# Optimization experiments

Hardware: AMD Instinct MI355X
Metric: run time of the kernel (lower is better)

The kernel has to match this reference:

```python
import jax, jax.numpy as jnp
import numpy as np
import math

B, N, D, H, O = 2, 1024, 256, 4, 8
DT, STEPS = 0.1, 5


def setup_inputs() -> dict:
    key = jax.random.key(0)
    ks = jax.random.split(key, 8)
    inv_d = 1.0 / math.sqrt(D)
    inv_ho = 1.0 / math.sqrt(H * O)
    return {
        "x": jax.random.normal(ks[0], (B, N, D), jnp.float32),
        "Wq": jax.random.normal(ks[1], (D, D), jnp.float32) * inv_d,
        "Wk": jax.random.normal(ks[2], (D, D), jnp.float32) * inv_d,
        "Wp": jax.random.normal(ks[3], (H * O, D), jnp.float32) * inv_d,
        "bp": jnp.zeros((H * O,), jnp.float32),
        "Wo": jax.random.normal(ks[4], (D, H * O), jnp.float32) * inv_ho,
        "bo": jnp.zeros((D,), jnp.float32),
        "omega": jax.random.normal(ks[5], (H, O), jnp.float32) * 0.1,
        "coupling_scale": jnp.asarray(1.0, jnp.float32),
    }


def reference(x, Wq, Wk, Wp, bp, Wo, bo, omega, coupling_scale):
    dk = D // H
    # attention coupling J_ij = softmax(q_i.k_j / sqrt(d_k))  -> (B,H,N,N)
    q = (x @ Wq.T).reshape(B, N, H, dk).transpose(0, 2, 1, 3)
    k = (x @ Wk.T).reshape(B, N, H, dk).transpose(0, 2, 1, 3)
    J = jax.nn.softmax(jnp.einsum('bhid,bhjd->bhij', q, k) / math.sqrt(dk), axis=-1)
    # initial phases (B,H,N,O)
    phases = (x @ Wp.T + bp).reshape(B, N, H, O).transpose(0, 2, 1, 3)
    om = omega[None, :, None, :]  # (1,H,1,O)

    def step(ph, _):
        # sum_j J_ij sin(phi_j - phi_i) = cos(phi_i)*(J@sin phi) - sin(phi_i)*(J@cos phi)
        s, c = jnp.sin(ph), jnp.cos(ph)
        coupling = c * jnp.einsum('bhij,bhjo->bhio', J, s) - s * jnp.einsum('bhij,bhjo->bhio', J, c)
        new = ph + DT * (om + coupling_scale * coupling)
        new = jnp.remainder(new + jnp.pi, 2 * jnp.pi) - jnp.pi
        return new, None

    phases, _ = jax.lax.scan(step, phases, None, length=STEPS)
    sig = jnp.cos(phases).transpose(0, 2, 1, 3).reshape(B, N, H * O)
    return sig @ Wo.T + bo
```

## Files before the change

kernel.cpp:

```cpp
#include <hip/hip_runtime.h>
#include <hip/hip_bf16.h>
#include <math.h>


#define NB 1024
#define NH 4
#define DD 256
#define NO 8
#define SCSZ 131072
#define PI_F      3.14159265358979323846f
#define TWO_PI_F  6.28318530717958647692f
#define INV_2PI_F 0.15915494309189533577f

typedef __attribute__((ext_vector_type(8))) short bf16x8;
typedef __attribute__((ext_vector_type(4))) float f32x4;
typedef unsigned long long u64;

__device__ __forceinline__ float b2f_u(unsigned short s) {
    union { unsigned u; float f; } x; x.u = ((unsigned)s) << 16; return x.f;
}
__device__ __forceinline__ unsigned short f2b(float f) {
    union { float f; unsigned u; } v; v.f = f;
    unsigned r = v.u + 0x7FFFu + ((v.u >> 16) & 1u);
    return (unsigned short)(r >> 16);
}
template<bool F32>
__device__ __forceinline__ uint4 load_pack8(const void* p, size_t off) {
    if (!F32) return *(const uint4*)((const unsigned short*)p + off);
    const float* fp = (const float*)p + off;
    float4 a = *(const float4*)fp;
    float4 b = *(const float4*)(fp + 4);
    uint4 r;
    r.x = (unsigned)f2b(a.x) | ((unsigned)f2b(a.y) << 16);
    r.y = (unsigned)f2b(a.z) | ((unsigned)f2b(a.w) << 16);
    r.z = (unsigned)f2b(b.x) | ((unsigned)f2b(b.y) << 16);
    r.w = (unsigned)f2b(b.z) | ((unsigned)f2b(b.w) << 16);
    return r;
}
__device__ __forceinline__ void load8_rt(int f32, const void* p, int i, float* f) {
    if (f32) {
        const float* fp = (const float*)p + i;
        float4 a = *(const float4*)fp;
        float4 b = *(const float4*)(fp + 4);
        f[0]=a.x; f[1]=a.y; f[2]=a.z; f[3]=a.w;
        f[4]=b.x; f[5]=b.y; f[6]=b.z; f[7]=b.w;
    } else {
        uint4 u = *(const uint4*)((const unsigned short*)p + i);
        f[0] = b2f_u(u.x & 0xFFFFu); f[1] = b2f_u(u.x >> 16);
        f[2] = b2f_u(u.y & 0xFFFFu); f[3] = b2f_u(u.y >> 16);
        f[4] = b2f_u(u.z & 0xFFFFu); f[5] = b2f_u(u.z >> 16);
        f[6] = b2f_u(u.w & 0xFFFFu); f[7] = b2f_u(u.w >> 16);
    }
}
__device__ __forceinline__ float read_cs_bf16(const void* p) {
    float vb = b2f_u(*(const unsigned short*)p);
    bool ok = isfinite(vb) && fabsf(vb) > 1e-30f && fabsf(vb) < 1e30f;
    if (ok) return vb;
    return *(const float*)p;
}
__device__ __forceinline__ int detect_inline(const unsigned short* x) {
    int l = threadIdx.x & 63;
    float a0 = fabsf(b2f_u(x[2 * l]));
    float a1 = fabsf(b2f_u(x[2 * (l + 64)]));
    unsigned long long b0 = __ballot(!(a0 >= 1e-10f && a0 <= 100.0f));
    unsigned long long b1 = __ballot(!(a1 >= 1e-10f && a1 <= 100.0f));
    return (__popcll(b0) + __popcll(b1)) > 16;
}
__device__ __forceinline__ void st8_llc(void* p, u64 v) {
    __hip_atomic_store((u64*)p, v, __ATOMIC_RELAXED, __HIP_MEMORY_SCOPE_AGENT);
}
__device__ __forceinline__ void st4_llc(unsigned* p, unsigned v) {
    __hip_atomic_store(p, v, __ATOMIC_RELAXED, __HIP_MEMORY_SCOPE_AGENT);
}
__device__ __forceinline__ void wait_flags64(const unsigned* f, unsigned tgt) {
    const int l = threadIdx.x & 63;
    unsigned spins = 0;
    for (;;) {
        unsigned v = __hip_atomic_load(f + l, __ATOMIC_RELAXED,
                                       __HIP_MEMORY_SCOPE_AGENT);
        if (__all((int)(v >= tgt))) break;
        __builtin_amdgcn_s_sleep(1);
        if (++spins > (1u << 18)) break;
    }
}
__device__ __forceinline__ void wait_flags_batch(const unsigned* f, unsigned tgt) {
    const int l = threadIdx.x & 63;
    unsigned spins = 0;
    for (;;) {
        unsigned a = __hip_atomic_load(f + l,       __ATOMIC_RELAXED, __HIP_MEMORY_SCOPE_AGENT);
        unsigned b = __hip_atomic_load(f + 64 + l,  __ATOMIC_RELAXED, __HIP_MEMORY_SCOPE_AGENT);
        unsigned c = __hip_atomic_load(f + 128 + l, __ATOMIC_RELAXED, __HIP_MEMORY_SCOPE_AGENT);
        unsigned d = __hip_atomic_load(f + 192 + l, __ATOMIC_RELAXED, __HIP_MEMORY_SCOPE_AGENT);
        unsigned m = min(min(a, b), min(c, d));
        if (__all((int)(m >= tgt))) break;
        __builtin_amdgcn_s_sleep(1);
        if (++spins > (1u << 18)) break;
    }
}

template<bool F32>
__device__ void projm_impl(
    const void* __restrict__ x, const void* __restrict__ Wq,
    const void* __restrict__ Wk, const void* __restrict__ Wp,
    const void* __restrict__ bp,
    unsigned short* __restrict__ Qb, unsigned short* __restrict__ Kb,
    float* __restrict__ PH, unsigned short* __restrict__ SC)
{
    __shared__ uint4 Xsh[64 * 32];
    __shared__ uint4 Wsh[64 * 32];
    const int tid = threadIdx.x;
    const int ftile = blockIdx.x % 9, itile = blockIdx.x / 9;
    const int i0 = itile * 64, f0 = ftile * 64;
    const int wave = tid >> 6, lane = tid & 63;
    const int n = lane & 15, quad = lane >> 4;

    #pragma unroll
    for (int g = 0; g < 8; g++) {
        int fidx = g * 256 + tid;
        int row = fidx >> 5, q = fidx & 31;
        int sw = (q & 24) | ((q ^ row) & 7);
        Xsh[row * 32 + sw] = load_pack8<F32>(x, (size_t)(i0 + row) * 256 + q * 8);
        int wr = f0 + row;
        uint4 wv = make_uint4(0, 0, 0, 0);
        if (wr < 256)      wv = load_pack8<F32>(Wq, (size_t)wr * 256 + q * 8);
        else if (wr < 512) wv = load_pack8<F32>(Wk, (size_t)(wr - 256) * 256 + q * 8);
        else if (wr < 544) wv = load_pack8<F32>(Wp, (size_t)(wr - 512) * 256 + q * 8);
        Wsh[row * 32 + sw] = wv;
    }
    __syncthreads();

    f32x4 acc[4];
    #pragma unroll
    for (int s = 0; s < 4; s++) acc[s] = (f32x4){0.f, 0.f, 0.f, 0.f};
    const int xrow = wave * 16 + n;
    #pragma unroll
    for (int s = 0; s < 8; s++) {
        int qc = s * 4 + quad;
        bf16x8 b = ((const bf16x8*)Xsh)[xrow * 32 + ((qc & 24) | ((qc ^ xrow) & 7))];
        #pragma unroll
        for (int sub = 0; sub < 4; sub++) {
            int wr = sub * 16 + n;
            bf16x8 a = ((const bf16x8*)Wsh)[wr * 32 + ((qc & 24) | ((qc ^ wr) & 7))];
            acc[sub] = __builtin_amdgcn_mfma_f32_16x16x32_bf16(a, b, acc[sub], 0, 0, 0);
        }
    }

    const int ig = i0 + wave * 16 + n;
    const int bb = ig >> 10, nr = ig & 1023;
    if (ftile < 4) {
        #pragma unroll
        for (int sub = 0; sub < 4; sub++) {
            int dd = sub * 16 + quad * 4;
            ushort4 v = make_ushort4(f2b(acc[sub][0] * 0.125f), f2b(acc[sub][1] * 0.125f),
                                     f2b(acc[sub][2] * 0.125f), f2b(acc[sub][3] * 0.125f));
            *(ushort4*)(Qb + ((size_t)((bb * NH + ftile) * NB + nr)) * 64 + dd) = v;
        }
    } else if (ftile < 8) {
        int h = ftile - 4;
        #pragma unroll
        for (int sub = 0; sub < 4; sub++) {
            int dd = sub * 16 + quad * 4;
            ushort4 v = make_ushort4(f2b(acc[sub][0]), f2b(acc[sub][1]),
                                     f2b(acc[sub][2]), f2b(acc[sub][3]));
            *(ushort4*)(Kb + ((size_t)((bb * NH + h) * NB + nr)) * 64 + dd) = v;
        }
    } else {
        #pragma unroll
        for (int sub = 0; sub < 2; sub++) {
            #pragma unroll
            for (int r = 0; r < 4; r++) {
                int fp = sub * 16 + quad * 4 + r;
                int h2 = fp >> 3, o = fp & 7;
                float bpv = F32 ? ((const float*)bp)[fp]
                                : b2f_u(((const unsigned short*)bp)[fp]);
                float v = acc[sub][r] + bpv;
                int bh = bb * NH + h2;
                PH[(size_t)bh * 8192 + o * 1024 + nr] = v;
                float sv, cv;
                __sincosf(v, &sv, &cv);
                SC[(size_t)(bh * 16 + o) * 1024 + nr]     = f2b(sv);
                SC[(size_t)(bh * 16 + 8 + o) * 1024 + nr] = f2b(cv);
            }
        }
    }
}

__global__ __launch_bounds__(256) void k_projm(
    const unsigned short* x, const void* Wq, const void* Wk, const void* Wp,
    const void* bp, unsigned short* Qb, unsigned short* Kb, float* PH,
    unsigned short* SC, unsigned int* flg)
{
    if (blockIdx.x == 0) {
        flg[threadIdx.x] = 0u;
        flg[threadIdx.x + 256] = 0u;
    }
    if (detect_inline(x)) projm_impl<true >(x, Wq, Wk, Wp, bp, Qb, Kb, PH, SC);
    else                  projm_impl<false>(x, Wq, Wk, Wp, bp, Qb, Kb, PH, SC);
}

__global__ __launch_bounds__(256) void k_mega4(
    const unsigned short* __restrict__ xraw,
    const unsigned short* __restrict__ Qb, const unsigned short* __restrict__ Kb,
    const float* __restrict__ PH0,
    unsigned short* __restrict__ SCB,
    const void* __restrict__ omega, const void* __restrict__ csp,
    const void* __restrict__ Wo, const void* __restrict__ bo,
    void* __restrict__ out, unsigned int* __restrict__ flg)
{
    __shared__ uint4 Ush[16 * 128];
    __shared__ f32x4 red[4][64];
    __shared__ float redS[4][16];
    __shared__ float Rsh[16];
    __shared__ float sig[4][32];

    const int tid = threadIdx.x;
    const int bid = blockIdx.x;
    const int bh  = bid >> 6;
    const int i0  = (bid & 63) * 16;
    const int wave = tid >> 6, lane = tid & 63;
    const int n = lane & 15, quad = lane >> 4;
    const int f32 = detect_inline(xraw);

    const unsigned short* qrow = Qb + ((size_t)(bh * NB) + i0 + n) * 64;
    bf16x8 bq0 = *(const bf16x8*)(qrow + quad * 8);
    bf16x8 bq1 = *(const bf16x8*)(qrow + 32 + quad * 8);
    float s = 0.f;
    const unsigned short* kbase = Kb + ((size_t)(bh * NB) + n) * 64;
    #pragma unroll
    for (int t = 0; t < 16; t++) {
        int jt = wave * 16 + t;
        const unsigned short* arow = kbase + (size_t)jt * 16 * 64;
        bf16x8 a0 = *(const bf16x8*)(arow + quad * 8);
        bf16x8 a1 = *(const bf16x8*)(arow + 32 + quad * 8);
        f32x4 acc = {0.f, 0.f, 0.f, 0.f};
        acc = __builtin_amdgcn_mfma_f32_16x16x32_bf16(a0, bq0, acc, 0, 0, 0);
        acc = __builtin_amdgcn_mfma_f32_16x16x32_bf16(a1, bq1, acc, 0, 0, 0);
        float u0 = __expf(acc[0]);
        float u1 = __expf(acc[1]);
        float u2 = __expf(acc[2]);
        float u3 = __expf(acc[3]);
        s += (u0 + u1) + (u2 + u3);
        ushort4 uv = make_ushort4(f2b(u0), f2b(u1), f2b(u2), f2b(u3));
        int cw = 2 * jt + (quad >> 1);
        ((ushort4*)Ush)[(n * 128 + (cw ^ (n & 7))) * 2 + (quad & 1)] = uv;
    }
    s += __shfl_xor(s, 16);
    s += __shfl_xor(s, 32);
    if (lane < 16) redS[wave][lane] = s;
    __syncthreads();
    if (tid < 16)
        Rsh[tid] = 1.0f / (redS[0][tid] + redS[1][tid] + redS[2][tid] + redS[3][tid]);

    float P[4];
    float cs_ = 0.f, om_ = 0.f;
    if (wave == 0 && n < 8) {
        const int o = n, h = bh & 3;
        cs_ = f32 ? *(const float*)csp : read_cs_bf16(csp);
        om_ = f32 ? ((const float*)omega)[h * NO + o]
                  : b2f_u(((const unsigned short*)omega)[h * NO + o]);
        float4 pv = *(const float4*)(PH0 + (size_t)bh * 8192 + o * 1024 + i0 + quad * 4);
        P[0] = pv.x; P[1] = pv.y; P[2] = pv.z; P[3] = pv.w;
    }

    #pragma unroll 1
    for (int k = 0; k < 5; k++) {
        const unsigned short* scrow = SCB + (size_t)k * SCSZ + (size_t)(bh * 16 + n) * 1024;
        unsigned short* scout       = SCB + (size_t)(k + 1) * SCSZ;
        f32x4 acc = {0.f, 0.f, 0.f, 0.f};
        #pragma unroll
        for (int t = 0; t < 8; t++) {
            int it = wave * 8 + t;
            bf16x8 a = ((const bf16x8*)Ush)[n * 128 + ((it * 4 + quad) ^ (n & 7))];
            bf16x8 b = *(const bf16x8*)(scrow + it * 32 + quad * 8);
            acc = __builtin_amdgcn_mfma_f32_16x16x32_bf16(a, b, acc, 0, 0, 0);
        }
        red[wave][lane] = acc;
        __syncthreads();

        if (wave == 0) {
            f32x4 a0 = red[0][lane], a1 = red[1][lane];
            f32x4 a2 = red[2][lane], a3 = red[3][lane];
            #pragma unroll
            for (int v = 0; v < 4; v++) acc[v] = (a0[v] + a1[v]) + (a2[v] + a3[v]);
            float C0 = __shfl_xor(acc[0], 8);
            float C1 = __shfl_xor(acc[1], 8);
            float C2 = __shfl_xor(acc[2], 8);
            float C3 = __shfl_xor(acc[3], 8);
            if (n < 8) {
                const int o = n;
                float S[4] = {acc[0], acc[1], acc[2], acc[3]};
                float C[4] = {C0, C1, C2, C3};
                float Rr[4] = {Rsh[quad * 4], Rsh[quad * 4 + 1],
                               Rsh[quad * 4 + 2], Rsh[quad * 4 + 3]};
                unsigned short sb[4], cb[4];
                #pragma unroll
                for (int r = 0; r < 4; r++) {
                    float si, ci;
                    __sincosf(P[r], &si, &ci);
                    float coup = (ci * S[r] - si * C[r]) * Rr[r];
                    float v = P[r] + 0.1f * (om_ + cs_ * coup);
                    float t2 = v + PI_F;
                    t2 -= floorf(t2 * INV_2PI_F) * TWO_PI_F;
                    P[r] = t2 - PI_F;
                    float sn, cn;
                    __sincosf(P[r], &sn, &cn);
                    sb[r] = f2b(sn); cb[r] = f2b(cn);
                }
                u64 sv = (u64)sb[0] | ((u64)sb[1] << 16) | ((u64)sb[2] << 32) | ((u64)sb[3] << 48);
                u64 cv = (u64)cb[0] | ((u64)cb[1] << 16) | ((u64)cb[2] << 32) | ((u64)cb[3] << 48);
                int i = i0 + quad * 4;
                st8_llc(scout + (size_t)(bh * 16 + o) * 1024 + i,     sv);
                st8_llc(scout + (size_t)(bh * 16 + 8 + o) * 1024 + i, cv);
            }
        }
        __syncthreads();
        if (tid == 0) st4_llc(&flg[bid], (unsigned)(k + 1));
        if (k < 4) {
            if (wave == 0) wait_flags64(&flg[bh * 64], (unsigned)(k + 1));
        } else {
            if (wave == 0) wait_flags_batch(&flg[(bid >> 8) * 256], 5u);
        }
        __syncthreads();
    }

    const unsigned short* scfin = SCB + (size_t)5 * SCSZ;
    const int ob = bid >> 8, n0 = (bid & 255) * 4;
    if (tid < 32) {
        int h = tid >> 3, o = tid & 7;
        u64 q = *(const u64*)(scfin + (size_t)((ob * NH + h) * 16 + 8 + o) * 1024 + n0);
        #pragma unroll
        for (int r = 0; r < 4; r++)
            sig[r][tid] = b2f_u((unsigned short)(q >> (16 * r)));
    }
    __syncthreads();
    float wv[32];
    #pragma unroll
    for (int d0 = 0; d0 < 32; d0 += 8) load8_rt(f32, Wo, tid * 32 + d0, wv + d0);
    const float bov = f32 ? ((const float*)bo)[tid] : b2f_u(((const unsigned short*)bo)[tid]);
    #pragma unroll
    for (int r = 0; r < 4; r++) {
        float acc = bov;
        #pragma unroll
        for (int t = 0; t < 32; t++) acc += sig[r][t] * wv[t];
        size_t oi = ((size_t)ob * 1024 + n0 + r) * DD + tid;
        if (f32) ((float*)out)[oi] = acc;
        else     ((unsigned short*)out)[oi] = f2b(acc);
    }
}

extern "C" void kernel_launch(void* const* d_in, const int* in_sizes, int n_in,
                              void* d_out, int out_size, void* d_ws, size_t ws_size,
                              hipStream_t stream)
{
    const unsigned short* x = (const unsigned short*)d_in[0];
    const void* Wq  = d_in[1];
    const void* Wk  = d_in[2];
    const void* Wp  = d_in[3];
    const void* bp  = d_in[4];
    const void* Wo  = d_in[5];
    const void* bo  = d_in[6];
    const void* om  = d_in[7];
    const void* cs  = d_in[8];

    char* w = (char*)d_ws;
    unsigned short* Qb  = (unsigned short*)w;
    unsigned short* Kb  = (unsigned short*)(w + (1u << 20));
    float*          PH0 = (float*)(w + (2u << 20));
    unsigned short* SCB = (unsigned short*)(w + (2u << 20) + (256u << 10));
    unsigned int*   flg = (unsigned int*)(w + (4u << 20));

    k_projm<<<288, 256, 0, stream>>>(x, Wq, Wk, Wp, bp, Qb, Kb, PH0, SCB, flg);
    k_mega4<<<512, 256, 0, stream>>>(x, Qb, Kb, PH0, SCB, om, cs,
                                     Wo, bo, d_out, flg);
}
```

Before: 127.3 us.

## Split output projection into separate kernel and streamline per-step flag sync

Moves the final output projection out of the persistent step kernel into a new k_out launch, so the last step no longer needs a grid-wide flag wait and can use plain stores. The per-step barrier now waits on vmcnt and has one lane publish the flag, polling inside the step branch instead of bracketing it with extra __syncthreads. This trades a software global barrier for an extra kernel launch boundary.

```diff
diff --git a/kernel.cpp b/kernel.cpp
--- a/kernel.cpp
+++ b/kernel.cpp
@@ -79,20 +79,6 @@
         unsigned v = __hip_atomic_load(f + l, __ATOMIC_RELAXED,
                                        __HIP_MEMORY_SCOPE_AGENT);
         if (__all((int)(v >= tgt))) break;
-        __builtin_amdgcn_s_sleep(1);
-        if (++spins > (1u << 18)) break;
-    }
-}
-__device__ __forceinline__ void wait_flags_batch(const unsigned* f, unsigned tgt) {
-    const int l = threadIdx.x & 63;
-    unsigned spins = 0;
-    for (;;) {
-        unsigned a = __hip_atomic_load(f + l,       __ATOMIC_RELAXED, __HIP_MEMORY_SCOPE_AGENT);
-        unsigned b = __hip_atomic_load(f + 64 + l,  __ATOMIC_RELAXED, __HIP_MEMORY_SCOPE_AGENT);
-        unsigned c = __hip_atomic_load(f + 128 + l, __ATOMIC_RELAXED, __HIP_MEMORY_SCOPE_AGENT);
-        unsigned d = __hip_atomic_load(f + 192 + l, __ATOMIC_RELAXED, __HIP_MEMORY_SCOPE_AGENT);
-        unsigned m = min(min(a, b), min(c, d));
-        if (__all((int)(m >= tgt))) break;
         __builtin_amdgcn_s_sleep(1);
         if (++spins > (1u << 18)) break;
     }
@@ -204,14 +190,12 @@
     const float* __restrict__ PH0,
     unsigned short* __restrict__ SCB,
     const void* __restrict__ omega, const void* __restrict__ csp,
-    const void* __restrict__ Wo, const void* __restrict__ bo,
-    void* __restrict__ out, unsigned int* __restrict__ flg)
+    unsigned int* __restrict__ flg)
 {
     __shared__ uint4 Ush[16 * 128];
     __shared__ f32x4 red[4][64];
     __shared__ float redS[4][16];
     __shared__ float Rsh[16];
-    __shared__ float sig[4][32];
 
     const int tid = threadIdx.x;
     const int bid = blockIdx.x;
@@ -309,19 +293,31 @@
                 u64 sv = (u64)sb[0] | ((u64)sb[1] << 16) | ((u64)sb[2] << 32) | ((u64)sb[3] << 48);
                 u64 cv = (u64)cb[0] | ((u64)cb[1] << 16) | ((u64)cb[2] << 32) | ((u64)cb[3] << 48);
                 int i = i0 + quad * 4;
-                st8_llc(scout + (size_t)(bh * 16 + o) * 1024 + i,     sv);
-                st8_llc(scout + (size_t)(bh * 16 + 8 + o) * 1024 + i, cv);
+                u64* ps = (u64*)(scout + (size_t)(bh * 16 + o) * 1024 + i);
+                u64* pc = (u64*)(scout + (size_t)(bh * 16 + 8 + o) * 1024 + i);
+                if (k < 4) { st8_llc(ps, sv); st8_llc(pc, cv); }
+                else       { *ps = sv;        *pc = cv; }
             }
-        }
-        __syncthreads();
-        if (tid == 0) st4_llc(&flg[bid], (unsigned)(k + 1));
-        if (k < 4) {
-            if (wave == 0) wait_flags64(&flg[bh * 64], (unsigned)(k + 1));
-        } else {
-            if (wave == 0) wait_flags_batch(&flg[(bid >> 8) * 256], 5u);
-        }
-        __syncthreads();
-    }
+            if (k < 4) {
+                asm volatile("s_waitcnt vmcnt(0)" ::: "memory");
+                if (lane == 0) st4_llc(&flg[bid], (unsigned)(k + 1));
+                wait_flags64(flg + bh * 64, (unsigned)(k + 1));
+            }
+        }
+        if (k < 4) __syncthreads();
+    }
+}
+
+__global__ __launch_bounds__(256) void k_out(
+    const unsigned short* __restrict__ xraw,
+    const unsigned short* __restrict__ SCB,
+    const void* __restrict__ Wo, const void* __restrict__ bo,
+    void* __restrict__ out)
+{
+    __shared__ float sig[4][32];
+    const int tid = threadIdx.x;
+    const int bid = blockIdx.x;
+    const int f32 = detect_inline(xraw);
 
     const unsigned short* scfin = SCB + (size_t)5 * SCSZ;
     const int ob = bid >> 8, n0 = (bid & 255) * 4;
@@ -370,6 +366,6 @@
     unsigned int*   flg = (unsigned int*)(w + (4u << 20));
 
     k_projm<<<288, 256, 0, stream>>>(x, Wq, Wk, Wp, bp, Qb, Kb, PH0, SCB, flg);
-    k_mega4<<<512, 256, 0, stream>>>(x, Qb, Kb, PH0, SCB, om, cs,
-                                     Wo, bo, d_out, flg);
-}
+    k_mega4<<<512, 256, 0, stream>>>(x, Qb, Kb, PH0, SCB, om, cs, flg);
+    k_out<<<512, 256, 0, stream>>>(x, SCB, Wo, bo, d_out);
+}
```

New measurement: 126.5 us. Within noise of the previous version (-0.6%).

## Narrow final-step flag wait and move flag signaling into the working wave

Applied to the files above, without the earlier changes.

The block-wide barrier before flag signaling is removed. The computing wave now drains its stores with s_waitcnt and publishes its own flag, then waits on the flags itself. At the last step it no longer waits for all 256 blocks of the batch, only for the four blocks (one per head) that produce the columns it reads. The sin store is also skipped at the final step because only cos is consumed afterward. The intent is to cut global synchronization latency. The risk is memory-ordering correctness, since only relaxed atomics plus a vmcnt wait are used.

```diff
diff --git a/kernel.cpp b/kernel.cpp
--- a/kernel.cpp
+++ b/kernel.cpp
@@ -79,20 +79,6 @@
         unsigned v = __hip_atomic_load(f + l, __ATOMIC_RELAXED,
                                        __HIP_MEMORY_SCOPE_AGENT);
         if (__all((int)(v >= tgt))) break;
-        __builtin_amdgcn_s_sleep(1);
-        if (++spins > (1u << 18)) break;
-    }
-}
-__device__ __forceinline__ void wait_flags_batch(const unsigned* f, unsigned tgt) {
-    const int l = threadIdx.x & 63;
-    unsigned spins = 0;
-    for (;;) {
-        unsigned a = __hip_atomic_load(f + l,       __ATOMIC_RELAXED, __HIP_MEMORY_SCOPE_AGENT);
-        unsigned b = __hip_atomic_load(f + 64 + l,  __ATOMIC_RELAXED, __HIP_MEMORY_SCOPE_AGENT);
-        unsigned c = __hip_atomic_load(f + 128 + l, __ATOMIC_RELAXED, __HIP_MEMORY_SCOPE_AGENT);
-        unsigned d = __hip_atomic_load(f + 192 + l, __ATOMIC_RELAXED, __HIP_MEMORY_SCOPE_AGENT);
-        unsigned m = min(min(a, b), min(c, d));
-        if (__all((int)(m >= tgt))) break;
         __builtin_amdgcn_s_sleep(1);
         if (++spins > (1u << 18)) break;
     }
@@ -309,16 +295,32 @@
                 u64 sv = (u64)sb[0] | ((u64)sb[1] << 16) | ((u64)sb[2] << 32) | ((u64)sb[3] << 48);
                 u64 cv = (u64)cb[0] | ((u64)cb[1] << 16) | ((u64)cb[2] << 32) | ((u64)cb[3] << 48);
                 int i = i0 + quad * 4;
-                st8_llc(scout + (size_t)(bh * 16 + o) * 1024 + i,     sv);
-                st8_llc(scout + (size_t)(bh * 16 + 8 + o) * 1024 + i, cv);
+                u64* ps = (u64*)(scout + (size_t)(bh * 16 + o) * 1024 + i);
+                u64* pc = (u64*)(scout + (size_t)(bh * 16 + 8 + o) * 1024 + i);
+                if (k < 4) st8_llc(ps, sv);
+                st8_llc(pc, cv);
             }
-        }
-        __syncthreads();
-        if (tid == 0) st4_llc(&flg[bid], (unsigned)(k + 1));
-        if (k < 4) {
-            if (wave == 0) wait_flags64(&flg[bh * 64], (unsigned)(k + 1));
-        } else {
-            if (wave == 0) wait_flags_batch(&flg[(bid >> 8) * 256], 5u);
+            asm volatile("s_waitcnt vmcnt(0)" ::: "memory");
+            if (lane == 0) st4_llc(&flg[bid], (unsigned)(k + 1));
+            if (k < 4) {
+                wait_flags64(flg + bh * 64, (unsigned)(k + 1));
+            } else {
+                const int jc = (bid & 255) >> 2;
+                const int ob = bid >> 8;
+                unsigned spins = 0;
+                for (;;) {
+                    int ok = 1;
+                    if (lane < 4) {
+                        unsigned v = __hip_atomic_load(
+                            &flg[(ob * 4 + lane) * 64 + jc],
+                            __ATOMIC_RELAXED, __HIP_MEMORY_SCOPE_AGENT);
+                        ok = (v >= 5u);
+                    }
+                    if (__all(ok)) break;
+                    __builtin_amdgcn_s_sleep(1);
+                    if (++spins > (1u << 18)) break;
+                }
+            }
         }
         __syncthreads();
     }
```

Result: slower. 130.0 us (+2.1%).
